# Kernel optimization log

Hardware: AMD Instinct MI355X
Metric: run time of the kernel (lower is better)

## Reference

```python
import jax, jax.numpy as jnp
import numpy as np

N_NODES = 100_000
N_EDGES = 1_000_000
LATENT = 64
HID_ATOM = 256
HID_BOND = 256
RBF_DIM = 32
RBF_DMAX = 10.0
N_ATOM_TYPES = 10
N_CHARGES = 6
N_BOND_ORDERS = 5


def setup_inputs() -> dict:
    key = jax.random.key(0)
    ks = jax.random.split(key, 12)
    positions = jax.random.normal(ks[0], (N_NODES, 3), dtype=jnp.float32) * 5.0
    quantized = jax.random.normal(ks[1], (N_NODES, LATENT), dtype=jnp.float32)
    pair_indices = jax.random.randint(ks[2], (N_EDGES, 2), 0, N_NODES, dtype=jnp.int64)
    s = 0.05
    return {
        "positions": positions,
        "quantized": quantized,
        "pair_indices": pair_indices,
        "aW1": jax.random.normal(ks[3], (LATENT, HID_ATOM), jnp.float32) * s,
        "ab1": jnp.zeros((HID_ATOM,), jnp.float32),
        "aW2": jax.random.normal(ks[4], (HID_ATOM, N_ATOM_TYPES + N_CHARGES), jnp.float32) * s,
        "ab2": jnp.zeros((N_ATOM_TYPES + N_CHARGES,), jnp.float32),
        "bW1": jax.random.normal(ks[5], (LATENT + RBF_DIM, HID_BOND), jnp.float32) * s,
        "bb1": jnp.zeros((HID_BOND,), jnp.float32),
        "bW2": jax.random.normal(ks[6], (HID_BOND, N_BOND_ORDERS), jnp.float32) * s,
        "bb2": jnp.zeros((N_BOND_ORDERS,), jnp.float32),
    }


def _norm_no_nan(x, eps=1e-8):
    # L2 norm over last axis, clamped to avoid NaN gradients at 0
    return jnp.sqrt(jnp.maximum(jnp.sum(x * x, axis=-1), eps))


def _rbf(D, D_min=0.0, D_max=RBF_DMAX, D_count=RBF_DIM):
    mu = jnp.linspace(D_min, D_max, D_count, dtype=D.dtype)  # [D_count]
    sigma = (D_max - D_min) / D_count
    z = (D[..., None] - mu) / sigma
    return jnp.exp(-z * z)  # [E, D_count]


def reference(positions, quantized, pair_indices, aW1, ab1, aW2, ab2, bW1, bb1, bW2, bb2):
    src = pair_indices[:, 0]
    dst = pair_indices[:, 1]
    # pairwise distances -> RBF expansion
    x_i = positions[src]            # [E, 3]
    x_j = positions[dst]
    dists = _rbf(_norm_no_nan(x_i - x_j))  # [E, rbf_dim]
    # atom decoder (per node)
    h = jax.nn.relu(quantized @ aW1 + ab1)
    scalar_logits = h @ aW2 + ab2
    atom_type_logits = scalar_logits[:, :N_ATOM_TYPES]
    atom_charge_logits = scalar_logits[:, N_ATOM_TYPES:]
    # bond decoder (per edge): gathered latent sum concat RBF
    pair_feats = quantized[src] + quantized[dst]           # [E, latent]
    combined = jnp.concatenate([pair_feats, dists], axis=1)  # [E, latent+rbf]
    hb = jax.nn.relu(combined @ bW1 + bb1)
    bond_order_logits = hb @ bW2 + bb2
    return (atom_type_logits, atom_charge_logits, bond_order_logits)
```

## Files before the change

### kernel.cpp

```cpp
#include <hip/hip_runtime.h>
#include <hip/hip_bf16.h>

typedef __bf16 bf16x8 __attribute__((ext_vector_type(8)));
typedef __bf16 bf16x4 __attribute__((ext_vector_type(4)));
typedef float  f32x4  __attribute__((ext_vector_type(4)));
typedef short  s16x4  __attribute__((ext_vector_type(4)));

#define N_NODES 100000
#define N_EDGES 1000000
#define LATENT  64
#define HID     256
#define RBF_DIM 32
#define NTYPES  10
#define NCHG    6
#define NBOND   5

#define ATOM_TILES (N_NODES / 32)
#define ANBLK 512

#define ETILE  32
#define ETILES (N_EDGES / ETILE)
#define ENBLK  768

static __device__ __forceinline__ f32x4 mfma16(bf16x4 a, bf16x4 b, f32x4 c) {
#if __has_builtin(__builtin_amdgcn_mfma_f32_16x16x16bf16_1k)
    s16x4 ai = __builtin_bit_cast(s16x4, a);
    s16x4 bi = __builtin_bit_cast(s16x4, b);
    return __builtin_amdgcn_mfma_f32_16x16x16bf16_1k(ai, bi, c, 0, 0, 0);
#else
    asm volatile("s_nop 1\n\t"
                 "v_mfma_f32_16x16x16_bf16 %0, %1, %2, %0\n\t"
                 "s_nop 7\n\ts_nop 7"
                 : "+v"(c) : "v"(a), "v"(b));
    return c;
#endif
}

struct __align__(16) ASmem {
    __bf16 qs[32][72];
    __bf16 hsE[32][264];
    float  red[4][2][4][64];
};

template<bool EMIT_QB>
__global__ __launch_bounds__(256, 2) void atom_kernel(
    const float* __restrict__ q,   const float* __restrict__ aW1,
    const float* __restrict__ ab1, const float* __restrict__ aW2,
    const float* __restrict__ ab2, float* __restrict__ outA,
    float* __restrict__ outB,      __bf16* __restrict__ qb)
{
    __shared__ ASmem sm;
    const int t    = threadIdx.x;
    const int w    = t >> 6;
    const int lane = t & 63;
    const int l15  = lane & 15;
    const int hi   = lane >> 4;
    const int wcol = w * 64;

    bf16x8 aw1f[2][4];
    #pragma unroll
    for (int kb = 0; kb < 2; ++kb)
        #pragma unroll
        for (int nt = 0; nt < 4; ++nt) {
            const int nn = wcol + nt * 16 + l15;
            const int k0 = kb * 32 + hi * 8;
            bf16x8 v;
            #pragma unroll
            for (int j = 0; j < 8; ++j) v[j] = (__bf16)aW1[(k0 + j) * HID + nn];
            aw1f[kb][nt] = v;
        }
    bf16x8 aw2f[2];
    #pragma unroll
    for (int kk = 0; kk < 2; ++kk) {
        const int k0 = (w * 2 + kk) * 32 + hi * 8;
        bf16x8 v;
        #pragma unroll
        for (int j = 0; j < 8; ++j) v[j] = (__bf16)aW2[(k0 + j) * 16 + l15];
        aw2f[kk] = v;
    }
    float4 b1v[4];
    #pragma unroll
    for (int nt = 0; nt < 4; ++nt)
        b1v[nt] = *(const float4*)(&ab1[wcol + nt * 16 + hi * 4]);

    const int m_st = t >> 3;
    const int p_st = t & 7;

    for (int tile = blockIdx.x; tile < ATOM_TILES; tile += ANBLK) {
        const int node0 = tile * 32;
        {
            const float* qr = q + (size_t)(node0 + m_st) * 64 + p_st * 8;
            const float4 a0 = *(const float4*)(qr);
            const float4 a1 = *(const float4*)(qr + 4);
            bf16x8 v;
            v[0] = (__bf16)a0.x; v[1] = (__bf16)a0.y; v[2] = (__bf16)a0.z; v[3] = (__bf16)a0.w;
            v[4] = (__bf16)a1.x; v[5] = (__bf16)a1.y; v[6] = (__bf16)a1.z; v[7] = (__bf16)a1.w;
            *(bf16x8*)(&sm.qs[m_st][p_st * 8]) = v;
            if constexpr (EMIT_QB)
                *(bf16x8*)(qb + (size_t)(node0 + m_st) * 64 + p_st * 8) = v;
        }
        __syncthreads();

        f32x4 acc[2][4];
        #pragma unroll
        for (int mt = 0; mt < 2; ++mt)
            #pragma unroll
            for (int nt = 0; nt < 4; ++nt)
                #pragma unroll
                for (int r = 0; r < 4; ++r)
                    acc[mt][nt][r] = ((const float*)&b1v[nt])[r];

        #pragma unroll
        for (int kb = 0; kb < 2; ++kb)
            #pragma unroll
            for (int mt = 0; mt < 2; ++mt) {
                const bf16x8 bq = *(const bf16x8*)((const char*)&sm.qs[0][0]
                                   + (mt * 16 + l15) * 144 + kb * 64 + hi * 16);
                #pragma unroll
                for (int nt = 0; nt < 4; ++nt)
                    acc[mt][nt] = __builtin_amdgcn_mfma_f32_16x16x32_bf16(
                        aw1f[kb][nt], bq, acc[mt][nt], 0, 0, 0);
            }

        #pragma unroll
        for (int mt = 0; mt < 2; ++mt)
            #pragma unroll
            for (int nt = 0; nt < 4; ++nt) {
                bf16x4 hv;
                #pragma unroll
                for (int r = 0; r < 4; ++r)
                    hv[r] = (__bf16)fmaxf(acc[mt][nt][r], 0.f);
                *(bf16x4*)(&sm.hsE[mt * 16 + l15][wcol + nt * 16 + hi * 4]) = hv;
            }
        __syncthreads();

        f32x4 acc2[2];
        {
            f32x4 z = {0.f, 0.f, 0.f, 0.f};
            acc2[0] = z; acc2[1] = z;
        }
        #pragma unroll
        for (int mt = 0; mt < 2; ++mt)
            #pragma unroll
            for (int kk = 0; kk < 2; ++kk) {
                const int kb = w * 2 + kk;
                const bf16x8 af = *(const bf16x8*)((const char*)&sm.hsE[0][0]
                                   + (mt * 16 + l15) * 528 + kb * 64 + hi * 16);
                acc2[mt] = __builtin_amdgcn_mfma_f32_16x16x32_bf16(
                    af, aw2f[kk], acc2[mt], 0, 0, 0);
            }
        #pragma unroll
        for (int mt = 0; mt < 2; ++mt)
            #pragma unroll
            for (int r = 0; r < 4; ++r)
                sm.red[w][mt][r][lane] = acc2[mt][r];
        __syncthreads();

        {
            const int o  = t & 15;
            const int m0 = t >> 4;
            #pragma unroll
            for (int half = 0; half < 2; ++half) {
                const int m  = m0 + half * 16;
                const int mt = m >> 4, rr = m & 15;
                const int hh = rr >> 2, r = rr & 3;
                float s = ab2[o];
                #pragma unroll
                for (int ww = 0; ww < 4; ++ww) s += sm.red[ww][mt][r][hh * 16 + o];
                const int node = node0 + m;
                if (o < NTYPES) outA[node * NTYPES + o] = s;
                else            outB[node * NCHG + (o - NTYPES)] = s;
            }
        }
        __syncthreads();
    }
}

struct __align__(16) ESmem {
    __bf16 comb[2][ETILE][104];
    float  red[2][4][2][4][64];
};

__device__ __forceinline__ void bar_lgkm() {
    asm volatile("s_waitcnt lgkmcnt(0)" ::: "memory");
    __builtin_amdgcn_s_barrier();
}

template<bool USEBF>
__global__ __launch_bounds__(256, 3) void edge_kernel(
    const float* __restrict__ pos, const float* __restrict__ qf,
    const __bf16* __restrict__ qb, const int* __restrict__ pair,
    const float* __restrict__ bW1, const float* __restrict__ bb1,
    const float* __restrict__ bW2, const float* __restrict__ bb2,
    float* __restrict__ outC)
{
    __shared__ ESmem sm;
    const int t    = threadIdx.x;
    const int w    = t >> 6;
    const int lane = t & 63;
    const int l15  = lane & 15;
    const int hi   = lane >> 4;
    const int hid0 = w * 64;

    bf16x8 bw1f[3][4];
    #pragma unroll
    for (int kb = 0; kb < 3; ++kb)
        #pragma unroll
        for (int nt = 0; nt < 4; ++nt) {
            const int nn = hid0 + nt * 16 + l15;
            const int k0 = kb * 32 + hi * 8;
            bf16x8 v;
            #pragma unroll
            for (int j = 0; j < 8; ++j) v[j] = (__bf16)bW1[(k0 + j) * HID + nn];
            bw1f[kb][nt] = v;
        }
    bf16x4 w2f[4];
    #pragma unroll
    for (int nt = 0; nt < 4; ++nt) {
        bf16x4 v;
        #pragma unroll
        for (int j = 0; j < 4; ++j)
            v[j] = (l15 < NBOND)
                 ? (__bf16)bW2[(hid0 + nt * 16 + hi * 4 + j) * NBOND + l15]
                 : (__bf16)0.f;
        w2f[nt] = v;
    }
    float4 b1v[4];
    #pragma unroll
    for (int nt = 0; nt < 4; ++nt)
        b1v[nt] = *(const float4*)(&bb1[hid0 + nt * 16 + hi * 4]);

    const int e_loc = t >> 3;
    const int p     = t & 7;

    int tile = blockIdx.x;
    bf16x8 gs, gd;
    float4 fs0, fs1, fd0, fd1;
    float  ps0, ps1, ps2, pd0, pd1, pd2;
    int2 pA = ((const int2*)pair)[(size_t)tile * ETILE + e_loc];
    #define GATHER(pN)                                                            \
        if constexpr (USEBF) {                                                    \
            gs = *(const bf16x8*)(qb + ((unsigned)(pN).x * 64u + (unsigned)(p*8)));\
            gd = *(const bf16x8*)(qb + ((unsigned)(pN).y * 64u + (unsigned)(p*8)));\
        } else {                                                                  \
            fs0 = *(const float4*)(qf + ((unsigned)(pN).x * 64u + (unsigned)(p*8)));     \
            fs1 = *(const float4*)(qf + ((unsigned)(pN).x * 64u + (unsigned)(p*8) + 4u));\
            fd0 = *(const float4*)(qf + ((unsigned)(pN).y * 64u + (unsigned)(p*8)));     \
            fd1 = *(const float4*)(qf + ((unsigned)(pN).y * 64u + (unsigned)(p*8) + 4u));\
        }                                                                         \
        ps0 = pos[(unsigned)(pN).x * 3u];  ps1 = pos[(unsigned)(pN).x * 3u + 1u]; \
        ps2 = pos[(unsigned)(pN).x * 3u + 2u];                                    \
        pd0 = pos[(unsigned)(pN).y * 3u];  pd1 = pos[(unsigned)(pN).y * 3u + 1u]; \
        pd2 = pos[(unsigned)(pN).y * 3u + 2u];

    #define STAGE(buf)                                                            \
        {                                                                         \
            bf16x8 cv;                                                            \
            if constexpr (USEBF) {                                                \
                _Pragma("unroll")                                                 \
                for (int j = 0; j < 8; ++j)                                       \
                    cv[j] = (__bf16)((float)gs[j] + (float)gd[j]);                \
            } else {                                                              \
                cv[0] = (__bf16)(fs0.x + fd0.x); cv[1] = (__bf16)(fs0.y + fd0.y); \
                cv[2] = (__bf16)(fs0.z + fd0.z); cv[3] = (__bf16)(fs0.w + fd0.w); \
                cv[4] = (__bf16)(fs1.x + fd1.x); cv[5] = (__bf16)(fs1.y + fd1.y); \
                cv[6] = (__bf16)(fs1.z + fd1.z); cv[7] = (__bf16)(fs1.w + fd1.w); \
            }                                                                     \
            *(bf16x8*)(&sm.comb[buf][e_loc][p * 8]) = cv;                         \
            const float dx = ps0 - pd0, dy = ps1 - pd1, dz = ps2 - pd2;           \
            const float D  = sqrtf(fmaxf(dx * dx + dy * dy + dz * dz, 1e-8f));    \
            bf16x4 rv;                                                            \
            _Pragma("unroll")                                                     \
            for (int j = 0; j < 4; ++j) {                                         \
                const float mu = (float)(p * 4 + j) * (10.0f / 31.0f);            \
                const float z  = (D - mu) * 3.2f;                                 \
                rv[j] = (__bf16)__expf(-z * z);                                   \
            }                                                                     \
            *(bf16x4*)(&sm.comb[buf][e_loc][64 + p * 4]) = rv;                    \
        }

    GATHER(pA);
    {
        const int tn = tile + ENBLK;
        pA = ((const int2*)pair)[(tn < ETILES ? (size_t)tn * ETILE : 0) + e_loc];
    }
    STAGE(0);
    GATHER(pA);
    {
        const int tn = tile + 2 * ENBLK;
        pA = ((const int2*)pair)[(tn < ETILES ? (size_t)tn * ETILE : 0) + e_loc];
    }
    bar_lgkm();

    int cur = 0;
    int e0_prev = -1;

    for (; tile < ETILES; tile += ENBLK) {
        const int e0 = tile * ETILE;

        if (e0_prev >= 0 && t < 160) {
            const int m = t / 5, o = t % 5;
            const int mt = m >> 4, rr = m & 15;
            const int hh = rr >> 2, r = rr & 3;
            float s = bb2[o];
            #pragma unroll
            for (int ww = 0; ww < 4; ++ww)
                s += sm.red[cur ^ 1][ww][mt][r][hh * 16 + o];
            outC[(size_t)(e0_prev + m) * NBOND + o] = s;
        }

        STAGE(cur ^ 1);

        GATHER(pA);
        {
            const int tn = tile + 3 * ENBLK;
            pA = ((const int2*)pair)[(tn < ETILES ? (size_t)tn * ETILE : 0) + e_loc];
        }

        f32x4 acc[2][4];
        #pragma unroll
        for (int mt = 0; mt < 2; ++mt)
            #pragma unroll
            for (int nt = 0; nt < 4; ++nt)
                #pragma unroll
                for (int r = 0; r < 4; ++r)
                    acc[mt][nt][r] = ((const float*)&b1v[nt])[r];

        #pragma unroll
        for (int kb = 0; kb < 3; ++kb)
            #pragma unroll
            for (int mt = 0; mt < 2; ++mt) {
                const bf16x8 bf = *(const bf16x8*)((const char*)&sm.comb[cur][0][0]
                                   + (mt * 16 + l15) * 208 + kb * 64 + hi * 16);
                #pragma unroll
                for (int nt = 0; nt < 4; ++nt)
                    acc[mt][nt] = __builtin_amdgcn_mfma_f32_16x16x32_bf16(
                        bw1f[kb][nt], bf, acc[mt][nt], 0, 0, 0);
            }

        {
            f32x4 acc2[2];
            {
                f32x4 z = {0.f, 0.f, 0.f, 0.f};
                acc2[0] = z; acc2[1] = z;
            }
            #pragma unroll
            for (int mt = 0; mt < 2; ++mt)
                #pragma unroll
                for (int nt = 0; nt < 4; ++nt) {
                    bf16x4 hv;
                    #pragma unroll
                    for (int r = 0; r < 4; ++r)
                        hv[r] = (__bf16)fmaxf(acc[mt][nt][r], 0.f);
                    acc2[mt] = mfma16(hv, w2f[nt], acc2[mt]);
                }
            #pragma unroll
            for (int mt = 0; mt < 2; ++mt)
                #pragma unroll
                for (int r = 0; r < 4; ++r)
                    sm.red[cur][w][mt][r][lane] = acc2[mt][r];
        }

        e0_prev = e0;
        bar_lgkm();
        cur ^= 1;
    }

    if (e0_prev >= 0 && t < 160) {
        const int m = t / 5, o = t % 5;
        const int mt = m >> 4, rr = m & 15;
        const int hh = rr >> 2, r = rr & 3;
        float s = bb2[o];
        #pragma unroll
        for (int ww = 0; ww < 4; ++ww)
            s += sm.red[cur ^ 1][ww][mt][r][hh * 16 + o];
        outC[(size_t)(e0_prev + m) * NBOND + o] = s;
    }
    #undef GATHER
    #undef STAGE
}

extern "C" void kernel_launch(void* const* d_in, const int* in_sizes, int n_in,
                              void* d_out, int out_size, void* d_ws, size_t ws_size,
                              hipStream_t stream)
{
    const float* pos = (const float*)d_in[0];
    const float* q   = (const float*)d_in[1];
    const int*   pair= (const int*)  d_in[2];
    const float* aW1 = (const float*)d_in[3];
    const float* ab1 = (const float*)d_in[4];
    const float* aW2 = (const float*)d_in[5];
    const float* ab2 = (const float*)d_in[6];
    const float* bW1 = (const float*)d_in[7];
    const float* bb1 = (const float*)d_in[8];
    const float* bW2 = (const float*)d_in[9];
    const float* bb2 = (const float*)d_in[10];

    float* out  = (float*)d_out;
    float* outA = out;
    float* outB = out + (size_t)N_NODES * NTYPES;
    float* outC = out + (size_t)N_NODES * (NTYPES + NCHG);

    const size_t qb_bytes = (size_t)N_NODES * LATENT * sizeof(__bf16);
    const bool use_bf = (ws_size >= qb_bytes);
    __bf16* qb = (__bf16*)d_ws;

    if (use_bf)
        hipLaunchKernelGGL(atom_kernel<true>, dim3(ANBLK), dim3(256), 0, stream,
                           q, aW1, ab1, aW2, ab2, outA, outB, qb);
    else
        hipLaunchKernelGGL(atom_kernel<false>, dim3(ANBLK), dim3(256), 0, stream,
                           q, aW1, ab1, aW2, ab2, outA, outB, qb);

    if (use_bf)
        hipLaunchKernelGGL(edge_kernel<true>, dim3(ENBLK), dim3(256), 0, stream,
                           pos, q, qb, pair, bW1, bb1, bW2, bb2, outC);
    else
        hipLaunchKernelGGL(edge_kernel<false>, dim3(ENBLK), dim3(256), 0, stream,
                           pos, q, qb, pair, bW1, bb1, bW2, bb2, outC);
}
```

Before: 100.7 us.

## Precompute edge distances in atom kernel and raise edge grid size

Edge distances are now computed at the end of the atom kernel and written to a workspace buffer. The edge kernel then reads one float per edge instead of gathering six scattered position values per thread, which cuts redundant gathers (previously each of the 8 threads per edge repeated them). The edge grid grows from 768 to 1280 blocks. The cost is an extra write and read of a 4 MB distance array, extra work in the atom kernel, and a larger workspace requirement; if the workspace is too small, the slower fp32 path is used.

```diff
diff --git a/kernel.cpp b/kernel.cpp
--- a/kernel.cpp
+++ b/kernel.cpp
@@ -20,7 +20,7 @@
 
 #define ETILE  32
 #define ETILES (N_EDGES / ETILE)
-#define ENBLK  768
+#define ENBLK  1280
 
 static __device__ __forceinline__ f32x4 mfma16(bf16x4 a, bf16x4 b, f32x4 c) {
 #if __has_builtin(__builtin_amdgcn_mfma_f32_16x16x16bf16_1k)
@@ -47,7 +47,9 @@
     const float* __restrict__ q,   const float* __restrict__ aW1,
     const float* __restrict__ ab1, const float* __restrict__ aW2,
     const float* __restrict__ ab2, float* __restrict__ outA,
-    float* __restrict__ outB,      __bf16* __restrict__ qb)
+    float* __restrict__ outB,      __bf16* __restrict__ qb,
+    const float* __restrict__ pos, const int* __restrict__ pair,
+    float* __restrict__ dist)
 {
     __shared__ ASmem sm;
     const int t    = threadIdx.x;
@@ -174,6 +176,16 @@
         }
         __syncthreads();
     }
+
+    if constexpr (EMIT_QB) {
+        for (int e = blockIdx.x * 256 + t; e < N_EDGES; e += ANBLK * 256) {
+            const int2 pr = ((const int2*)pair)[e];
+            const float dx = pos[(unsigned)pr.x * 3u]      - pos[(unsigned)pr.y * 3u];
+            const float dy = pos[(unsigned)pr.x * 3u + 1u] - pos[(unsigned)pr.y * 3u + 1u];
+            const float dz = pos[(unsigned)pr.x * 3u + 2u] - pos[(unsigned)pr.y * 3u + 2u];
+            dist[e] = sqrtf(fmaxf(dx * dx + dy * dy + dz * dz, 1e-8f));
+        }
+    }
 }
 
 struct __align__(16) ESmem {
@@ -189,7 +201,8 @@
 template<bool USEBF>
 __global__ __launch_bounds__(256, 3) void edge_kernel(
     const float* __restrict__ pos, const float* __restrict__ qf,
-    const __bf16* __restrict__ qb, const int* __restrict__ pair,
+    const __bf16* __restrict__ qb, const float* __restrict__ dist,
+    const int* __restrict__ pair,
     const float* __restrict__ bW1, const float* __restrict__ bb1,
     const float* __restrict__ bW2, const float* __restrict__ bb2,
     float* __restrict__ outC)
@@ -235,40 +248,44 @@
 
     int tile = blockIdx.x;
     bf16x8 gs, gd;
+    float  Dv;
     float4 fs0, fs1, fd0, fd1;
     float  ps0, ps1, ps2, pd0, pd1, pd2;
-    int2 pA = ((const int2*)pair)[(size_t)tile * ETILE + e_loc];
-    #define GATHER(pN)                                                            \
+
+    #define GATHER(pN, tg)                                                        \
         if constexpr (USEBF) {                                                    \
             gs = *(const bf16x8*)(qb + ((unsigned)(pN).x * 64u + (unsigned)(p*8)));\
             gd = *(const bf16x8*)(qb + ((unsigned)(pN).y * 64u + (unsigned)(p*8)));\
+            Dv = dist[(size_t)(tg) * ETILE + e_loc];                              \
         } else {                                                                  \
             fs0 = *(const float4*)(qf + ((unsigned)(pN).x * 64u + (unsigned)(p*8)));     \
             fs1 = *(const float4*)(qf + ((unsigned)(pN).x * 64u + (unsigned)(p*8) + 4u));\
             fd0 = *(const float4*)(qf + ((unsigned)(pN).y * 64u + (unsigned)(p*8)));     \
             fd1 = *(const float4*)(qf + ((unsigned)(pN).y * 64u + (unsigned)(p*8) + 4u));\
-        }                                                                         \
-        ps0 = pos[(unsigned)(pN).x * 3u];  ps1 = pos[(unsigned)(pN).x * 3u + 1u]; \
-        ps2 = pos[(unsigned)(pN).x * 3u + 2u];                                    \
-        pd0 = pos[(unsigned)(pN).y * 3u];  pd1 = pos[(unsigned)(pN).y * 3u + 1u]; \
-        pd2 = pos[(unsigned)(pN).y * 3u + 2u];
+            ps0 = pos[(unsigned)(pN).x * 3u];  ps1 = pos[(unsigned)(pN).x * 3u + 1u];    \
+            ps2 = pos[(unsigned)(pN).x * 3u + 2u];                                \
+            pd0 = pos[(unsigned)(pN).y * 3u];  pd1 = pos[(unsigned)(pN).y * 3u + 1u];    \
+            pd2 = pos[(unsigned)(pN).y * 3u + 2u];                                \
+        }
 
     #define STAGE(buf)                                                            \
         {                                                                         \
             bf16x8 cv;                                                            \
+            float D;                                                              \
             if constexpr (USEBF) {                                                \
                 _Pragma("unroll")                                                 \
                 for (int j = 0; j < 8; ++j)                                       \
                     cv[j] = (__bf16)((float)gs[j] + (float)gd[j]);                \
+                D = Dv;                                                           \
             } else {                                                              \
                 cv[0] = (__bf16)(fs0.x + fd0.x); cv[1] = (__bf16)(fs0.y + fd0.y); \
                 cv[2] = (__bf16)(fs0.z + fd0.z); cv[3] = (__bf16)(fs0.w + fd0.w); \
                 cv[4] = (__bf16)(fs1.x + fd1.x); cv[5] = (__bf16)(fs1.y + fd1.y); \
                 cv[6] = (__bf16)(fs1.z + fd1.z); cv[7] = (__bf16)(fs1.w + fd1.w); \
+                const float dx = ps0 - pd0, dy = ps1 - pd1, dz = ps2 - pd2;       \
+                D = sqrtf(fmaxf(dx * dx + dy * dy + dz * dz, 1e-8f));             \
             }                                                                     \
             *(bf16x8*)(&sm.comb[buf][e_loc][p * 8]) = cv;                         \
-            const float dx = ps0 - pd0, dy = ps1 - pd1, dz = ps2 - pd2;           \
-            const float D  = sqrtf(fmaxf(dx * dx + dy * dy + dz * dz, 1e-8f));    \
             bf16x4 rv;                                                            \
             _Pragma("unroll")                                                     \
             for (int j = 0; j < 4; ++j) {                                         \
@@ -279,17 +296,15 @@
             *(bf16x4*)(&sm.comb[buf][e_loc][64 + p * 4]) = rv;                    \
         }
 
-    GATHER(pA);
-    {
-        const int tn = tile + ENBLK;
-        pA = ((const int2*)pair)[(tn < ETILES ? (size_t)tn * ETILE : 0) + e_loc];
-    }
+    int  tgA = tile;
+    int2 pA  = ((const int2*)pair)[(size_t)tile * ETILE + e_loc];
+    GATHER(pA, tgA);
+    tgA = (tile + ENBLK < ETILES) ? tile + ENBLK : 0;
+    pA  = ((const int2*)pair)[(size_t)tgA * ETILE + e_loc];
     STAGE(0);
-    GATHER(pA);
-    {
-        const int tn = tile + 2 * ENBLK;
-        pA = ((const int2*)pair)[(tn < ETILES ? (size_t)tn * ETILE : 0) + e_loc];
-    }
+    GATHER(pA, tgA);
+    tgA = (tile + 2 * ENBLK < ETILES) ? tile + 2 * ENBLK : 0;
+    pA  = ((const int2*)pair)[(size_t)tgA * ETILE + e_loc];
     bar_lgkm();
 
     int cur = 0;
@@ -311,11 +326,9 @@
 
         STAGE(cur ^ 1);
 
-        GATHER(pA);
-        {
-            const int tn = tile + 3 * ENBLK;
-            pA = ((const int2*)pair)[(tn < ETILES ? (size_t)tn * ETILE : 0) + e_loc];
-        }
+        GATHER(pA, tgA);
+        tgA = (tile + 3 * ENBLK < ETILES) ? tile + 3 * ENBLK : 0;
+        pA  = ((const int2*)pair)[(size_t)tgA * ETILE + e_loc];
 
         f32x4 acc[2][4];
         #pragma unroll
@@ -401,21 +414,23 @@
     float* outB = out + (size_t)N_NODES * NTYPES;
     float* outC = out + (size_t)N_NODES * (NTYPES + NCHG);
 
-    const size_t qb_bytes = (size_t)N_NODES * LATENT * sizeof(__bf16);
-    const bool use_bf = (ws_size >= qb_bytes);
-    __bf16* qb = (__bf16*)d_ws;
+    const size_t qb_bytes   = (size_t)N_NODES * LATENT * sizeof(__bf16);
+    const size_t dist_bytes = (size_t)N_EDGES * sizeof(float);
+    const bool use_bf = (ws_size >= qb_bytes + dist_bytes);
+    __bf16* qb   = (__bf16*)d_ws;
+    float*  dist = (float*)((char*)d_ws + qb_bytes);
 
     if (use_bf)
         hipLaunchKernelGGL(atom_kernel<true>, dim3(ANBLK), dim3(256), 0, stream,
-                           q, aW1, ab1, aW2, ab2, outA, outB, qb);
+                           q, aW1, ab1, aW2, ab2, outA, outB, qb, pos, pair, dist);
     else
         hipLaunchKernelGGL(atom_kernel<false>, dim3(ANBLK), dim3(256), 0, stream,
-                           q, aW1, ab1, aW2, ab2, outA, outB, qb);
+                           q, aW1, ab1, aW2, ab2, outA, outB, qb, pos, pair, dist);
 
     if (use_bf)
         hipLaunchKernelGGL(edge_kernel<true>, dim3(ENBLK), dim3(256), 0, stream,
-                           pos, q, qb, pair, bW1, bb1, bW2, bb2, outC);
+                           pos, q, qb, dist, pair, bW1, bb1, bW2, bb2, outC);
     else
         hipLaunchKernelGGL(edge_kernel<false>, dim3(ENBLK), dim3(256), 0, stream,
-                           pos, q, qb, pair, bW1, bb1, bW2, bb2, outC);
+                           pos, q, qb, dist, pair, bW1, bb1, bW2, bb2, outC);
 }
```

Result: slower. 113.3 us (+12.5%).
